# Performance work log

Measured on AMD Instinct MI355X. Metric: run time of the kernel, lower is better.

Reference implementation:

```python
import jax, jax.numpy as jnp
import numpy as np

B, N, NPOINT, NSAMPLE = 8, 4096, 1024, 32
IN_CH = 29
MLP = [64, 64, 128]
D_IN = IN_CH + 3  # 32
D_OUT = 128
EPS = 1e-5


def setup_inputs() -> dict:
    key = jax.random.key(0)
    ks = jax.random.split(key, 32)
    inp = {}
    inp["xyz"] = jax.random.normal(ks[0], (B, 3, N), jnp.float32)
    inp["points"] = jax.random.normal(ks[1], (B, IN_CH, N), jnp.float32)
    last = IN_CH + 3
    for i, oc in enumerate(MLP):
        inp[f"mlp_w{i}"] = jax.random.normal(ks[2 + i], (oc, last), jnp.float32) * np.sqrt(2.0 / last).astype(np.float32)
        inp[f"mlp_b{i}"] = jnp.zeros((oc,), jnp.float32)
        inp[f"mlp_g{i}"] = jnp.ones((oc,), jnp.float32)
        inp[f"mlp_be{i}"] = jnp.zeros((oc,), jnp.float32)
        last = oc
    inp["conv1_w"] = jax.random.normal(ks[10], (D_OUT // 2, 4), jnp.float32) * np.float32(np.sqrt(2.0 / 4))
    inp["conv1_b"] = jnp.zeros((D_OUT // 2,), jnp.float32)
    inp["bn1_g"] = jnp.ones((D_OUT // 2,), jnp.float32)
    inp["bn1_be"] = jnp.zeros((D_OUT // 2,), jnp.float32)
    inp["conv2_w"] = jax.random.normal(ks[11], (D_OUT // 2, D_IN), jnp.float32) * np.float32(np.sqrt(2.0 / D_IN))
    inp["conv2_b"] = jnp.zeros((D_OUT // 2,), jnp.float32)
    inp["bn2_g"] = jnp.ones((D_OUT // 2,), jnp.float32)
    inp["bn2_be"] = jnp.zeros((D_OUT // 2,), jnp.float32)
    return inp


def _conv1x1(x, w, b):
    # x: [B,Cin,ns,S], w: [Cout,Cin] -> [B,Cout,ns,S]
    return jnp.einsum("bcns,oc->bons", x, w) + b[None, :, None, None]


def _bn_relu(x, g, be):
    # training-mode BatchNorm2d: batch stats over (B, ns, S), biased variance
    m = jnp.mean(x, axis=(0, 2, 3), keepdims=True)
    v = jnp.var(x, axis=(0, 2, 3), keepdims=True)
    y = g[None, :, None, None] * (x - m) * jax.lax.rsqrt(v + EPS) + be[None, :, None, None]
    return jax.nn.relu(y)


def _fps(xyz):
    # xyz: [B,N,3] -> centroid indices [B,NPOINT]; deterministic start at index 0
    Bn, Nn, _ = xyz.shape

    def step(carry, _):
        dist, far = carry
        cen = jnp.take_along_axis(xyz, far[:, None, None], axis=1)  # [B,1,3]
        d = jnp.sum((xyz - cen) ** 2, axis=-1)                      # [B,N]
        dist = jnp.minimum(dist, d)
        new_far = jnp.argmax(dist, axis=-1).astype(jnp.int32)
        return (dist, new_far), far

    init = (jnp.full((Bn, Nn), 1e10, xyz.dtype), jnp.zeros((Bn,), jnp.int32))
    _, cents = jax.lax.scan(step, init, None, length=NPOINT)
    return cents.T  # [B,NPOINT]


def _forward(xyz, points, mlp_params, conv1_w, conv1_b, bn1_g, bn1_be,
             conv2_w, conv2_b, bn2_g, bn2_be):
    xyz_t = xyz.transpose(0, 2, 1)      # [B,N,3]
    pts_t = points.transpose(0, 2, 1)   # [B,N,C]
    xyz_sg = jax.lax.stop_gradient(xyz_t)

    ct_idx = _fps(xyz_sg)                                   # [B,S]
    bidx = jnp.arange(B)[:, None]
    ct_xyz = xyz_t[bidx, ct_idx]                            # [B,S,3]

    # kNN via squared distances (indices only -> stop_gradient)
    ct_sg = jax.lax.stop_gradient(ct_xyz)
    d2 = (jnp.sum(ct_sg ** 2, -1)[:, :, None]
          + jnp.sum(xyz_sg ** 2, -1)[:, None, :]
          - 2.0 * jnp.einsum("bsc,bnc->bsn", ct_sg, xyz_sg))  # [B,S,N]
    _, gidx = jax.lax.top_k(-d2, NSAMPLE)                     # [B,S,ns]

    bidx3 = jnp.arange(B)[:, None, None]
    grouped_xyz = xyz_t[bidx3, gidx]                          # [B,S,ns,3]
    ft_xyz = grouped_xyz - ct_xyz[:, :, None, :]              # [B,S,ns,3]
    ft_points = jnp.concatenate([ft_xyz, pts_t[bidx3, gidx]], axis=-1)  # [B,S,ns,3+C]
    ft = ft_points.transpose(0, 3, 2, 1)                      # [B,3+C,ns,S]

    # shared MLP (conv-bn-relu stack), then max over neighbors
    x = ft
    for (w, b, g, be) in mlp_params:
        x = _bn_relu(_conv1x1(x, w, b), g, be)
    new_points1 = jnp.max(x, axis=2)                          # [B,mlp[-1],S]

    # relative positional encoding branch
    ct_p = ct_xyz.transpose(0, 2, 1)                          # [B,3,S]
    grouped_p = grouped_xyz.transpose(0, 3, 2, 1)             # [B,3,ns,S]
    rel = grouped_p - ct_p[:, :, None, :]                     # [B,3,ns,S]
    rd = jnp.sqrt(jnp.maximum(jnp.sum(rel ** 2, axis=1, keepdims=True), 1e-12))
    new_xyz = _bn_relu(_conv1x1(jnp.concatenate([rel, rd], axis=1), conv1_w, conv1_b), bn1_g, bn1_be)
    new_pts = _bn_relu(_conv1x1(ft, conv2_w, conv2_b), bn2_g, bn2_be)

    f_concat = jnp.concatenate([new_xyz, new_pts], axis=1)    # [B,d_out,ns,S]
    new_points2 = jnp.concatenate([jnp.mean(f_concat, axis=2), jnp.max(f_concat, axis=2)], axis=1)
    conv_points = jnp.concatenate([new_points1, new_points2], axis=1)  # [B,mlp[-1]+2*d_out,S]
    return ct_p, conv_points


def reference(xyz, points,
              mlp_w0, mlp_b0, mlp_g0, mlp_be0,
              mlp_w1, mlp_b1, mlp_g1, mlp_be1,
              mlp_w2, mlp_b2, mlp_g2, mlp_be2,
              conv1_w, conv1_b, bn1_g, bn1_be,
              conv2_w, conv2_b, bn2_g, bn2_be):
    mlp_params = [(mlp_w0, mlp_b0, mlp_g0, mlp_be0),
                  (mlp_w1, mlp_b1, mlp_g1, mlp_be1),
                  (mlp_w2, mlp_b2, mlp_g2, mlp_be2)]
    return _forward(xyz, points, mlp_params, conv1_w, conv1_b, bn1_g, bn1_be,
                    conv2_w, conv2_b, bn2_g, bn2_be)
```

## Files before the change

### kernel.cpp

```cpp
#include <hip/hip_runtime.h>
#include <cfloat>
#include <math.h>

constexpr int B_ = 8, N_ = 4096, S_ = 1024, NS_ = 32;
constexpr int R_ = B_ * S_ * NS_;
constexpr float EPS_ = 1e-5f;

__device__ __forceinline__ unsigned dpp_red_umax(unsigned x) {
    unsigned t;
#define STEP_(ctrl) t = (unsigned)__builtin_amdgcn_update_dpp((int)x, (int)x, ctrl, 0xf, 0xf, false); x = x > t ? x : t;
    STEP_(0x111) STEP_(0x112) STEP_(0x114) STEP_(0x118) STEP_(0x142) STEP_(0x143)
#undef STEP_
    return x;
}
__device__ __forceinline__ void dpp_min_u64(unsigned& hi, unsigned& lo) {
#define STEP_(ctrl) { \
    unsigned h2 = (unsigned)__builtin_amdgcn_update_dpp((int)hi, (int)hi, ctrl, 0xf, 0xf, false); \
    unsigned l2 = (unsigned)__builtin_amdgcn_update_dpp((int)lo, (int)lo, ctrl, 0xf, 0xf, false); \
    if (h2 < hi || (h2 == hi && l2 < lo)) { hi = h2; lo = l2; } }
    STEP_(0x111) STEP_(0x112) STEP_(0x114) STEP_(0x118) STEP_(0x142) STEP_(0x143)
#undef STEP_
}
__device__ __forceinline__ float dpp_sum_f32(float x) {
#define ADD_(ctrl, rm) { \
    int t_ = __builtin_amdgcn_update_dpp(0, __float_as_int(x), ctrl, rm, 0xf, true); \
    x += __int_as_float(t_); }
    ADD_(0x111, 0xf) ADD_(0x112, 0xf) ADD_(0x114, 0xf) ADD_(0x118, 0xf)
    ADD_(0x142, 0xa) ADD_(0x143, 0xc)
#undef ADD_
    return x;
}

__global__ __launch_bounds__(256) void fps_kernel(const float* __restrict__ xyz,
                                                  int* __restrict__ ct_idx) {
    int b = blockIdx.x;
    const float* xb = xyz + (size_t)b * 3 * N_;
    int t = threadIdx.x;
    __shared__ float sx[N_], sy[N_], sz[N_];
    __shared__ unsigned long long sb[2][4];
    for (int i = t; i < N_; i += 256) {
        sx[i] = xb[i];
        sy[i] = xb[N_ + i];
        sz[i] = xb[2 * N_ + i];
    }
    float px[16], py[16], pz[16], dist[16];
#pragma unroll
    for (int j = 0; j < 16; j++) {
        int n = t * 16 + j;
        px[j] = xb[n];
        py[j] = xb[N_ + n];
        pz[j] = xb[2 * N_ + n];
        dist[j] = 1e10f;
    }
    __syncthreads();
    float cx = sx[0], cy = sy[0], cz = sz[0];
    int far = 0;
    int w = t >> 6;
    for (int it = 0; it < S_; it++) {
        if (t == 0) ct_idx[b * S_ + it] = far;
#pragma unroll
        for (int j = 0; j < 16; j++) {
            float dx = px[j] - cx, dy = py[j] - cy, dz = pz[j] - cz;
            float d = dx * dx;
            d = fmaf(dy, dy, d);
            d = fmaf(dz, dz, d);
            dist[j] = fminf(dist[j], d);
        }
        float v8[8], v4[4], v2[2];
        int j8[8], j4[4], j2[2];
#pragma unroll
        for (int j = 0; j < 8; j++) {
            bool ge = dist[2 * j] >= dist[2 * j + 1];
            v8[j] = ge ? dist[2 * j] : dist[2 * j + 1];
            j8[j] = ge ? 2 * j : 2 * j + 1;
        }
#pragma unroll
        for (int j = 0; j < 4; j++) {
            bool ge = v8[2 * j] >= v8[2 * j + 1];
            v4[j] = ge ? v8[2 * j] : v8[2 * j + 1];
            j4[j] = ge ? j8[2 * j] : j8[2 * j + 1];
        }
#pragma unroll
        for (int j = 0; j < 2; j++) {
            bool ge = v4[2 * j] >= v4[2 * j + 1];
            v2[j] = ge ? v4[2 * j] : v4[2 * j + 1];
            j2[j] = ge ? j4[2 * j] : j4[2 * j + 1];
        }
        bool ge0 = v2[0] >= v2[1];
        float lmax = ge0 ? v2[0] : v2[1];
        int jbest = ge0 ? j2[0] : j2[1];
        unsigned wm = (unsigned)__builtin_amdgcn_readlane(
            (int)dpp_red_umax(__float_as_uint(lmax)), 63);
        unsigned long long lanes = __ballot(__float_as_uint(lmax) == wm);
        int l = __ffsll(lanes) - 1;
        int js = __builtin_amdgcn_readlane(jbest, l);
        unsigned n = (unsigned)(((w << 6) + l) * 16 + js);
        int p = it & 1;
        if ((t & 63) == 0)
            sb[p][w] = ((unsigned long long)wm << 32) | (unsigned)~n;
        __syncthreads();
        unsigned long long b0 = sb[p][0], b1 = sb[p][1], b2 = sb[p][2], b3 = sb[p][3];
        unsigned long long ma = b0 > b1 ? b0 : b1;
        unsigned long long mb = b2 > b3 ? b2 : b3;
        unsigned long long bw = ma > mb ? ma : mb;
        far = (int)(~(unsigned)(bw & 0xffffffffu)) & (N_ - 1);
        cx = sx[far]; cy = sy[far]; cz = sz[far];
    }
}

__global__ __launch_bounds__(256) void knn_kernel(const float* __restrict__ xyz,
                                                  const int* __restrict__ ct_idx,
                                                  int* __restrict__ gidx) {
    int bs = blockIdx.x;
    int b = bs >> 10;
    const float* xb = xyz + (size_t)b * 3 * N_;
    int ci = ct_idx[bs];
    float cx = xb[ci], cy = xb[N_ + ci], cz = xb[2 * N_ + ci];
    float cs = cx * cx + cy * cy + cz * cz;
    int t = threadIdx.x;
    unsigned long long pk[16];
#pragma unroll
    for (int j = 0; j < 16; j++) {
        int n = j * 256 + t;
        float x = xb[n], y = xb[N_ + n], z = xb[2 * N_ + n];
        float xn = x * x + y * y + z * z;
        float dot = cx * x + cy * y + cz * z;
        float val = cs + xn - 2.f * dot;
        unsigned vb = __float_as_uint(val);
        unsigned key = (vb & 0x80000000u) ? ~vb : (vb | 0x80000000u);
        pk[j] = ((unsigned long long)key << 32) | (unsigned)n;
    }
    __shared__ unsigned long long sw[2][4];
    int out_base = bs * NS_;
    int w = t >> 6;
    for (int iter = 0; iter < NS_; iter++) {
        unsigned long long m8[8], m4[4];
#pragma unroll
        for (int j = 0; j < 8; j++) m8[j] = pk[2 * j] < pk[2 * j + 1] ? pk[2 * j] : pk[2 * j + 1];
#pragma unroll
        for (int j = 0; j < 4; j++) m4[j] = m8[2 * j] < m8[2 * j + 1] ? m8[2 * j] : m8[2 * j + 1];
        unsigned long long ma = m4[0] < m4[1] ? m4[0] : m4[1];
        unsigned long long mb = m4[2] < m4[3] ? m4[2] : m4[3];
        unsigned long long best = ma < mb ? ma : mb;
        unsigned hi = (unsigned)(best >> 32), lo = (unsigned)best;
        dpp_min_u64(hi, lo);
        int p = iter & 1;
        if ((t & 63) == 63) sw[p][w] = ((unsigned long long)hi << 32) | lo;
        __syncthreads();
        unsigned long long b0 = sw[p][0], b1 = sw[p][1], b2 = sw[p][2], b3 = sw[p][3];
        unsigned long long wa = b0 < b1 ? b0 : b1;
        unsigned long long wb = b2 < b3 ? b2 : b3;
        unsigned long long bw = wa < wb ? wa : wb;
        int n = (int)(unsigned)(bw & 0xffffffffu);
        if (t == 0) gidx[out_base + iter] = n;
        if ((n & 255) == t) pk[n >> 8] = 0xFFFFFFFF00000000ull | (unsigned)n;
    }
}

__global__ __launch_bounds__(256) void ctp_kernel(const float* __restrict__ xyz,
                                                  const int* __restrict__ ct_idx,
                                                  float* __restrict__ out) {
    int i = blockIdx.x * 256 + threadIdx.x;
    if (i >= B_ * 3 * S_) return;
    int b = i / (3 * S_);
    int rem = i - b * 3 * S_;
    int c = rem >> 10;
    int s = rem & (S_ - 1);
    int ci = ct_idx[b * S_ + s];
    out[i] = xyz[(size_t)b * 3 * N_ + (size_t)c * N_ + ci];
}

__global__ __launch_bounds__(256) void gather_kernel(const float* __restrict__ xyz,
                                                     const float* __restrict__ pts,
                                                     const int* __restrict__ ct_idx,
                                                     const int* __restrict__ gidx,
                                                     float* __restrict__ ft) {
    int r = blockIdx.x * 256 + threadIdx.x;
    int b = r >> 15;
    int s = (r >> 5) & (S_ - 1);
    int g = gidx[r];
    int ci = ct_idx[b * S_ + s];
    const float* xb = xyz + (size_t)b * 3 * N_;
    float rx = xb[g] - xb[ci];
    float ry = xb[N_ + g] - xb[N_ + ci];
    float rz = xb[2 * N_ + g] - xb[2 * N_ + ci];
    ft[r] = rx;
    ft[(size_t)R_ + r] = ry;
    ft[(size_t)2 * R_ + r] = rz;
    float rd = sqrtf(fmaxf(rx * rx + ry * ry + rz * rz, 1e-12f));
    ft[(size_t)32 * R_ + r] = rd;
    const float* pb = pts + (size_t)b * 29 * N_;
#pragma unroll
    for (int c = 0; c < 29; c++) ft[(size_t)(3 + c) * R_ + r] = pb[(size_t)c * N_ + g];
}

template <int CIN, bool AFF>
__global__ __launch_bounds__(256) void convk(const float* __restrict__ xin,
                                             const float* __restrict__ W,
                                             const float* __restrict__ bias,
                                             const float* __restrict__ ab,
                                             float* __restrict__ out0,
                                             float* __restrict__ out1,
                                             float* __restrict__ partial) {
    __shared__ float Ws[CIN][64];
    __shared__ float bs_[64];
    __shared__ float as_[CIN], bbs[CIN];
    __shared__ float red[4][64][2];
    int oc0 = blockIdx.y * 64;
    for (int i = threadIdx.x; i < CIN * 64; i += 256) {
        int o = i & 63, c = i >> 6;
        Ws[c][o] = W[(size_t)(oc0 + o) * CIN + c];
    }
    if (threadIdx.x < 64) bs_[threadIdx.x] = bias[oc0 + threadIdx.x];
    if (AFF) {
        for (int i = threadIdx.x; i < CIN; i += 256) { as_[i] = ab[i]; bbs[i] = ab[CIN + i]; }
    }
    __syncthreads();
    size_t r0 = (size_t)blockIdx.x * 512 + threadIdx.x;
    float acc0[64], acc1[64];
#pragma unroll
    for (int o = 0; o < 64; o++) { acc0[o] = 0.f; acc1[o] = 0.f; }
    for (int c = 0; c < CIN; c++) {
        float x0 = xin[(size_t)c * R_ + r0];
        float x1 = xin[(size_t)c * R_ + r0 + 256];
        if (AFF) {
            float a = as_[c], bb = bbs[c];
            x0 = fmaxf(fmaf(a, x0, bb), 0.f);
            x1 = fmaxf(fmaf(a, x1, bb), 0.f);
        }
#pragma unroll
        for (int o = 0; o < 64; o++) {
            float w = Ws[c][o];
            acc0[o] = fmaf(x0, w, acc0[o]);
            acc1[o] = fmaf(x1, w, acc1[o]);
        }
    }
    float* outp = blockIdx.y ? out1 : out0;
    int wv = threadIdx.x >> 6;
#pragma unroll
    for (int o = 0; o < 64; o++) {
        float bv = bs_[o];
        float y0 = acc0[o] + bv;
        float y1 = acc1[o] + bv;
        outp[(size_t)o * R_ + r0] = y0;
        outp[(size_t)o * R_ + r0 + 256] = y1;
        float s = y0 + y1;
        float q = fmaf(y0, y0, y1 * y1);
        s = dpp_sum_f32(s);
        q = dpp_sum_f32(q);
        if ((threadIdx.x & 63) == 63) { red[wv][o][0] = s; red[wv][o][1] = q; }
    }
    __syncthreads();
    if (threadIdx.x < 64) {
        int o = threadIdx.x;
        float s = red[0][o][0] + red[1][o][0] + red[2][o][0] + red[3][o][0];
        float q = red[0][o][1] + red[1][o][1] + red[2][o][1] + red[3][o][1];
        partial[(size_t)(oc0 + o) * 1024 + blockIdx.x] = s;
        partial[(size_t)(oc0 + o) * 1024 + 512 + blockIdx.x] = q;
    }
}

__global__ __launch_bounds__(256) void conv1_kernel(const float* __restrict__ ft,
                                                    const float* __restrict__ W,
                                                    const float* __restrict__ bias,
                                                    float* __restrict__ out,
                                                    float* __restrict__ partial) {
    __shared__ float Ws[4][64];
    __shared__ float bs_[64];
    __shared__ float red[4][64][2];
    {
        int i = threadIdx.x;
        if (i < 256) { int o = i & 63, c = i >> 6; Ws[c][o] = W[o * 4 + c]; }
    }
    if (threadIdx.x < 64) bs_[threadIdx.x] = bias[threadIdx.x];
    __syncthreads();
    size_t r0 = (size_t)blockIdx.x * 512 + threadIdx.x;
    float acc0[64], acc1[64];
#pragma unroll
    for (int o = 0; o < 64; o++) { acc0[o] = 0.f; acc1[o] = 0.f; }
    const int chs[4] = {0, 1, 2, 32};
#pragma unroll
    for (int c = 0; c < 4; c++) {
        int ch = chs[c];
        float x0 = ft[(size_t)ch * R_ + r0];
        float x1 = ft[(size_t)ch * R_ + r0 + 256];
#pragma unroll
        for (int o = 0; o < 64; o++) {
            float w = Ws[c][o];
            acc0[o] = fmaf(x0, w, acc0[o]);
            acc1[o] = fmaf(x1, w, acc1[o]);
        }
    }
    int wv = threadIdx.x >> 6;
#pragma unroll
    for (int o = 0; o < 64; o++) {
        float bv = bs_[o];
        float y0 = acc0[o] + bv;
        float y1 = acc1[o] + bv;
        out[(size_t)o * R_ + r0] = y0;
        out[(size_t)o * R_ + r0 + 256] = y1;
        float s = y0 + y1;
        float q = fmaf(y0, y0, y1 * y1);
        s = dpp_sum_f32(s);
        q = dpp_sum_f32(q);
        if ((threadIdx.x & 63) == 63) { red[wv][o][0] = s; red[wv][o][1] = q; }
    }
    __syncthreads();
    if (threadIdx.x < 64) {
        int o = threadIdx.x;
        float s = red[0][o][0] + red[1][o][0] + red[2][o][0] + red[3][o][0];
        float q = red[0][o][1] + red[1][o][1] + red[2][o][1] + red[3][o][1];
        partial[(size_t)o * 1024 + blockIdx.x] = s;
        partial[(size_t)o * 1024 + 512 + blockIdx.x] = q;
    }
}

__global__ __launch_bounds__(64) void statsf(const float* __restrict__ partial,
                                             const float* __restrict__ g,
                                             const float* __restrict__ be,
                                             float* __restrict__ ab, int C) {
    int c = blockIdx.x, t = threadIdx.x;
    float s = 0.f, q = 0.f;
    for (int i = t; i < 512; i += 64) {
        s += partial[(size_t)c * 1024 + i];
        q += partial[(size_t)c * 1024 + 512 + i];
    }
    s = dpp_sum_f32(s);
    q = dpp_sum_f32(q);
    if (t == 63) {
        float inv = 1.0f / (float)R_;
        float mean = s * inv;
        float var = q * inv - mean * mean;
        float a = g[c] / sqrtf(var + EPS_);
        ab[c] = a;
        ab[C + c] = be[c] - mean * a;
    }
}

__global__ __launch_bounds__(128) void final_max(const float* __restrict__ yA,
                                                 const float* __restrict__ yC,
                                                 const float* __restrict__ ab,
                                                 float* __restrict__ out) {
    int bs = blockIdx.x;
    int c = threadIdx.x;
    const float* src = (c < 64 ? yA + (size_t)c * R_ : yC + (size_t)(c - 64) * R_) + (size_t)bs * NS_;
    float a = ab[c], bb = ab[128 + c];
    const float4* s4 = reinterpret_cast<const float4*>(src);
    float m = -FLT_MAX;
#pragma unroll
    for (int i = 0; i < 8; i++) {
        float4 v = s4[i];
        m = fmaxf(m, fmaxf(fmaf(a, v.x, bb), 0.f));
        m = fmaxf(m, fmaxf(fmaf(a, v.y, bb), 0.f));
        m = fmaxf(m, fmaxf(fmaf(a, v.z, bb), 0.f));
        m = fmaxf(m, fmaxf(fmaf(a, v.w, bb), 0.f));
    }
    int b = bs >> 10, s = bs & (S_ - 1);
    out[24576 + (size_t)b * 393216 + (size_t)c * 1024 + s] = m;
}

__global__ __launch_bounds__(128) void final_meanmax(const float* __restrict__ z1,
                                                     const float* __restrict__ z2,
                                                     const float* __restrict__ ab1,
                                                     const float* __restrict__ ab2,
                                                     float* __restrict__ out) {
    int bs = blockIdx.x;
    int c = threadIdx.x;
    const float* src;
    float a, bb;
    if (c < 64) { src = z1 + (size_t)c * R_; a = ab1[c]; bb = ab1[64 + c]; }
    else        { src = z2 + (size_t)(c - 64) * R_; a = ab2[c - 64]; bb = ab2[64 + (c - 64)]; }
    src += (size_t)bs * NS_;
    const float4* s4 = reinterpret_cast<const float4*>(src);
    float m = -FLT_MAX, sm = 0.f;
#pragma unroll
    for (int i = 0; i < 8; i++) {
        float4 v = s4[i];
        float t0 = fmaxf(fmaf(a, v.x, bb), 0.f); sm += t0; m = fmaxf(m, t0);
        float t1 = fmaxf(fmaf(a, v.y, bb), 0.f); sm += t1; m = fmaxf(m, t1);
        float t2 = fmaxf(fmaf(a, v.z, bb), 0.f); sm += t2; m = fmaxf(m, t2);
        float t3 = fmaxf(fmaf(a, v.w, bb), 0.f); sm += t3; m = fmaxf(m, t3);
    }
    int b = bs >> 10, s = bs & (S_ - 1);
    size_t ob = 24576 + (size_t)b * 393216;
    out[ob + (size_t)(128 + c) * 1024 + s] = sm * 0.03125f;
    out[ob + (size_t)(256 + c) * 1024 + s] = m;
}

extern "C" void kernel_launch(void* const* d_in, const int* in_sizes, int n_in,
                              void* d_out, int out_size, void* d_ws, size_t ws_size,
                              hipStream_t stream) {
    const float* xyz = (const float*)d_in[0];
    const float* pts = (const float*)d_in[1];
    const float* W0 = (const float*)d_in[2];  const float* b0 = (const float*)d_in[3];
    const float* g0 = (const float*)d_in[4];  const float* be0 = (const float*)d_in[5];
    const float* W1 = (const float*)d_in[6];  const float* b1 = (const float*)d_in[7];
    const float* g1 = (const float*)d_in[8];  const float* be1 = (const float*)d_in[9];
    const float* W2 = (const float*)d_in[10]; const float* b2 = (const float*)d_in[11];
    const float* g2 = (const float*)d_in[12]; const float* be2 = (const float*)d_in[13];
    const float* c1w = (const float*)d_in[14]; const float* c1b = (const float*)d_in[15];
    const float* bg1 = (const float*)d_in[16]; const float* bbe1 = (const float*)d_in[17];
    const float* c2w = (const float*)d_in[18]; const float* c2b = (const float*)d_in[19];
    const float* bg2 = (const float*)d_in[20]; const float* bbe2 = (const float*)d_in[21];
    float* out = (float*)d_out;

    int* ct_idx = (int*)d_ws;
    int* gidx = ct_idx + B_ * S_;
    float* fbase = (float*)d_ws;
    float* ft = fbase + 270336;
    float* A = ft + (size_t)33 * R_;
    float* Bb = A + (size_t)64 * R_;
    float* C = Bb + (size_t)64 * R_;
    float* partial = C + (size_t)64 * R_;
    float* ab0 = partial + 131072;
    float* ab1 = ab0 + 128;
    float* ab2 = ab1 + 128;
    float* abz1 = ab2 + 256;
    float* abz2 = abz1 + 128;

    fps_kernel<<<B_, 256, 0, stream>>>(xyz, ct_idx);
    knn_kernel<<<B_ * S_, 256, 0, stream>>>(xyz, ct_idx, gidx);
    ctp_kernel<<<(B_ * 3 * S_ + 255) / 256, 256, 0, stream>>>(xyz, ct_idx, out);
    gather_kernel<<<R_ / 256, 256, 0, stream>>>(xyz, pts, ct_idx, gidx, ft);

    convk<32, false><<<dim3(R_ / 512, 1), 256, 0, stream>>>(ft, W0, b0, nullptr, A, nullptr, partial);
    statsf<<<64, 64, 0, stream>>>(partial, g0, be0, ab0, 64);
    convk<64, true><<<dim3(R_ / 512, 1), 256, 0, stream>>>(A, W1, b1, ab0, Bb, nullptr, partial);
    statsf<<<64, 64, 0, stream>>>(partial, g1, be1, ab1, 64);
    convk<64, true><<<dim3(R_ / 512, 2), 256, 0, stream>>>(Bb, W2, b2, ab1, A, C, partial);
    statsf<<<128, 64, 0, stream>>>(partial, g2, be2, ab2, 128);
    final_max<<<B_ * S_, 128, 0, stream>>>(A, C, ab2, out);

    convk<32, false><<<dim3(R_ / 512, 1), 256, 0, stream>>>(ft, c2w, c2b, nullptr, Bb, nullptr, partial);
    statsf<<<64, 64, 0, stream>>>(partial, bg2, bbe2, abz2, 64);

    conv1_kernel<<<R_ / 512, 256, 0, stream>>>(ft, c1w, c1b, A, partial);
    statsf<<<64, 64, 0, stream>>>(partial, bg1, bbe1, abz1, 64);

    final_meanmax<<<B_ * S_, 128, 0, stream>>>(A, Bb, abz1, abz2, out);
}
```

Before: 1.513 ms.

## Streamline FPS argmax with min-index DPP reduction and float4 centroid loads

```diff
diff --git a/kernel.cpp b/kernel.cpp
--- a/kernel.cpp
+++ b/kernel.cpp
@@ -9,6 +9,13 @@
 __device__ __forceinline__ unsigned dpp_red_umax(unsigned x) {
     unsigned t;
 #define STEP_(ctrl) t = (unsigned)__builtin_amdgcn_update_dpp((int)x, (int)x, ctrl, 0xf, 0xf, false); x = x > t ? x : t;
+    STEP_(0x111) STEP_(0x112) STEP_(0x114) STEP_(0x118) STEP_(0x142) STEP_(0x143)
+#undef STEP_
+    return x;
+}
+__device__ __forceinline__ unsigned dpp_red_umin(unsigned x) {
+    unsigned t;
+#define STEP_(ctrl) t = (unsigned)__builtin_amdgcn_update_dpp((int)x, (int)x, ctrl, 0xf, 0xf, false); x = x < t ? x : t;
     STEP_(0x111) STEP_(0x112) STEP_(0x114) STEP_(0x118) STEP_(0x142) STEP_(0x143)
 #undef STEP_
     return x;
@@ -36,76 +43,71 @@
     int b = blockIdx.x;
     const float* xb = xyz + (size_t)b * 3 * N_;
     int t = threadIdx.x;
-    __shared__ float sx[N_], sy[N_], sz[N_];
+    __shared__ float4 sp[N_];
+    __shared__ int sct[S_];
     __shared__ unsigned long long sb[2][4];
     for (int i = t; i < N_; i += 256) {
-        sx[i] = xb[i];
-        sy[i] = xb[N_ + i];
-        sz[i] = xb[2 * N_ + i];
+        float x = xb[i], y = xb[N_ + i], z = xb[2 * N_ + i];
+        sp[i] = make_float4(x, y, z, 0.f);
     }
     float px[16], py[16], pz[16], dist[16];
+    unsigned idxr[16];
 #pragma unroll
     for (int j = 0; j < 16; j++) {
-        int n = t * 16 + j;
+        int n = j * 256 + t;
         px[j] = xb[n];
         py[j] = xb[N_ + n];
         pz[j] = xb[2 * N_ + n];
         dist[j] = 1e10f;
-    }
-    __syncthreads();
-    float cx = sx[0], cy = sy[0], cz = sz[0];
+        idxr[j] = (unsigned)n;
+    }
+    __syncthreads();
+    float4 c4 = sp[0];
     int far = 0;
     int w = t >> 6;
     for (int it = 0; it < S_; it++) {
-        if (t == 0) ct_idx[b * S_ + it] = far;
+        if (t == 0) sct[it] = far;
 #pragma unroll
         for (int j = 0; j < 16; j++) {
-            float dx = px[j] - cx, dy = py[j] - cy, dz = pz[j] - cz;
+            float dx = px[j] - c4.x, dy = py[j] - c4.y, dz = pz[j] - c4.z;
             float d = dx * dx;
             d = fmaf(dy, dy, d);
             d = fmaf(dz, dz, d);
             dist[j] = fminf(dist[j], d);
         }
-        float v8[8], v4[4], v2[2];
-        int j8[8], j4[4], j2[2];
-#pragma unroll
-        for (int j = 0; j < 8; j++) {
-            bool ge = dist[2 * j] >= dist[2 * j + 1];
-            v8[j] = ge ? dist[2 * j] : dist[2 * j + 1];
-            j8[j] = ge ? 2 * j : 2 * j + 1;
-        }
-#pragma unroll
-        for (int j = 0; j < 4; j++) {
-            bool ge = v8[2 * j] >= v8[2 * j + 1];
-            v4[j] = ge ? v8[2 * j] : v8[2 * j + 1];
-            j4[j] = ge ? j8[2 * j] : j8[2 * j + 1];
-        }
-#pragma unroll
-        for (int j = 0; j < 2; j++) {
-            bool ge = v4[2 * j] >= v4[2 * j + 1];
-            v2[j] = ge ? v4[2 * j] : v4[2 * j + 1];
-            j2[j] = ge ? j4[2 * j] : j4[2 * j + 1];
-        }
-        bool ge0 = v2[0] >= v2[1];
-        float lmax = ge0 ? v2[0] : v2[1];
-        int jbest = ge0 ? j2[0] : j2[1];
+        float v8[8], v4[4];
+#pragma unroll
+        for (int j = 0; j < 8; j++) v8[j] = fmaxf(dist[2 * j], dist[2 * j + 1]);
+#pragma unroll
+        for (int j = 0; j < 4; j++) v4[j] = fmaxf(v8[2 * j], v8[2 * j + 1]);
+        float lmax = fmaxf(fmaxf(v4[0], v4[1]), fmaxf(v4[2], v4[3]));
         unsigned wm = (unsigned)__builtin_amdgcn_readlane(
             (int)dpp_red_umax(__float_as_uint(lmax)), 63);
-        unsigned long long lanes = __ballot(__float_as_uint(lmax) == wm);
-        int l = __ffsll(lanes) - 1;
-        int js = __builtin_amdgcn_readlane(jbest, l);
-        unsigned n = (unsigned)(((w << 6) + l) * 16 + js);
+        unsigned c8[8], c4i[4];
+#pragma unroll
+        for (int j = 0; j < 8; j++) {
+            unsigned a = (__float_as_uint(dist[2 * j]) == wm) ? idxr[2 * j] : 0xffffffffu;
+            unsigned bq = (__float_as_uint(dist[2 * j + 1]) == wm) ? idxr[2 * j + 1] : 0xffffffffu;
+            c8[j] = a < bq ? a : bq;
+        }
+#pragma unroll
+        for (int j = 0; j < 4; j++) c4i[j] = c8[2 * j] < c8[2 * j + 1] ? c8[2 * j] : c8[2 * j + 1];
+        unsigned c01 = c4i[0] < c4i[1] ? c4i[0] : c4i[1];
+        unsigned c23 = c4i[2] < c4i[3] ? c4i[2] : c4i[3];
+        unsigned mn = dpp_red_umin(c01 < c23 ? c01 : c23);
         int p = it & 1;
-        if ((t & 63) == 0)
-            sb[p][w] = ((unsigned long long)wm << 32) | (unsigned)~n;
+        if ((t & 63) == 63)
+            sb[p][w] = ((unsigned long long)wm << 32) | (unsigned)~mn;
         __syncthreads();
         unsigned long long b0 = sb[p][0], b1 = sb[p][1], b2 = sb[p][2], b3 = sb[p][3];
         unsigned long long ma = b0 > b1 ? b0 : b1;
         unsigned long long mb = b2 > b3 ? b2 : b3;
         unsigned long long bw = ma > mb ? ma : mb;
         far = (int)(~(unsigned)(bw & 0xffffffffu)) & (N_ - 1);
-        cx = sx[far]; cy = sy[far]; cz = sz[far];
-    }
+        c4 = sp[far];
+    }
+    __syncthreads();
+    for (int i = t; i < S_; i += 256) ct_idx[b * S_ + i] = sct[i];
 }
 
 __global__ __launch_bounds__(256) void knn_kernel(const float* __restrict__ xyz,
```

After: 1.467 ms. 1.03x faster.
